# Kernel tuning notes

Hardware: AMD Instinct MI355X
Metric: run time of the kernel (lower is better)

Reference implementation:

```python
import jax, jax.numpy as jnp
import numpy as np

# 8 corner offsets of the trilinear cell: (8, 3)
_OFFS = jnp.array([[i, j, k] for i in (0, 1) for j in (0, 1) for k in (0, 1)], dtype=jnp.int32)


def _gridding(cloud, R):
    """Trilinear scatter of points into an RxRxR occupancy-weight grid.

    cloud: (b, n, 3) with coords in [-0.5, 0.5] (already divided by scale).
    Returns (b, R, R, R) grid where each point adds trilinear weights to its
    8 neighboring cells (the GRNet gridding_distance forward kernel).
    """
    b, n, _ = cloud.shape
    v = (cloud + 0.5) * R                      # continuous voxel coords in [0, R)
    lower = jnp.floor(v)
    frac = v - lower                           # (b, n, 3) in [0, 1)
    lower = lower.astype(jnp.int32)
    nb = lower[:, :, None, :] + _OFFS[None, None]              # (b, n, 8, 3)
    # per-axis trilinear weight: (1 - frac) for the low corner, frac for the high
    w_d = jnp.where(_OFFS[None, None] == 0,
                    1.0 - frac[:, :, None, :], frac[:, :, None, :])  # (b, n, 8, 3)
    w = jnp.prod(w_d, axis=-1)                                  # (b, n, 8)
    valid = jnp.all((nb >= 0) & (nb < R), axis=-1)              # (b, n, 8)
    w = jnp.where(valid, w, 0.0)
    nbc = jnp.clip(nb, 0, R - 1)
    flat = (nbc[..., 0] * R + nbc[..., 1]) * R + nbc[..., 2]    # (b, n, 8)
    batch_off = jnp.arange(b, dtype=jnp.int32)[:, None, None] * (R * R * R)
    idx = (flat + batch_off).reshape(-1)
    grid = jnp.zeros((b * R * R * R,), cloud.dtype).at[idx].add(w.reshape(-1))
    return grid.reshape(b, R, R, R)


def setup_inputs() -> dict:
    key = jax.random.key(0)
    k1, k2 = jax.random.split(key)
    R = 128
    B, N1, N2 = 16, 65536, 65536
    # coords in [-(R-2)/2, (R-2)/2] so that after /scale they are inside (-0.5, 0.5)
    pred = (jax.random.uniform(k1, (B, N1, 3), jnp.float32) - 0.5) * (R - 2)
    gt = (jax.random.uniform(k2, (B, N2, 3), jnp.float32) - 0.5) * (R - 2)
    return {"pred_cloud": pred, "gt_cloud": gt, "scale": R}


def reference(pred_cloud, gt_cloud, scale):
    pred = pred_cloud / scale
    gt = gt_cloud / scale
    return _gridding(pred, scale), _gridding(gt, scale)
```

## Files before the change

kernel.cpp:

```cpp
#include <hip/hip_runtime.h>
#include <stdint.h>


constexpr int R    = 128;
constexpr int R3c  = R * R * R;
constexpr int BPG  = 256;
constexpr int NBLK = 512;
constexpr int BLKT = 512;
constexpr int CAP  = 4096;
constexpr int MAXBINS = 8192;

constexpr size_t WS_CNT    = 0;
constexpr size_t WS_BUCKET = 1u << 20;

typedef float f4v __attribute__((ext_vector_type(4)));

__device__ __forceinline__ uint32_t quant1(float p) {
    const float S = 16384.0f;
    const uint32_t QMAX = (126u << 14) | 16383u;
    float v = p + 64.0f;
    return min(__float2uint_rn(fmaxf(v, 0.0f) * S), QMAX);
}

__device__ __forceinline__ uint2 pack_rec(uint32_t xq, uint32_t yq, uint32_t zq) {
    return make_uint2(xq | (yq << 21), (yq >> 11) | (zq << 10));
}
__device__ __forceinline__ void unpack_rec(uint2 r, uint32_t& xq, uint32_t& yq, uint32_t& zq) {
    xq = r.x & 0x1FFFFFu;
    yq = (r.x >> 21) | ((r.y & 0x3FFu) << 11);
    zq = (r.y >> 10) & 0x1FFFFFu;
}

__device__ __forceinline__ void load_point(
    const float* __restrict__ pred, const float* __restrict__ gt,
    int i, int total1, int n1, int n2, int B,
    float& px, float& py, float& pz, int& cb)
{
    const float* p;
    if (i < total1) { p = pred + (size_t)i * 3; cb = i / n1; }
    else { int j = i - total1; p = gt + (size_t)j * 3; cb = B + j / n2; }
    px = p[0]; py = p[1]; pz = p[2];
}

__device__ __forceinline__ void region_range(uint32_t xq, uint32_t yq, uint32_t zq,
                                             int& rx0, int& rx1, int& ry0, int& ry1,
                                             int& rz0, int& rz1)
{
    int ix = xq >> 14, iy = yq >> 14, iz = zq >> 14;
    rx0 = ix >> 4; rx1 = (ix + 1) >> 4;
    ry0 = iy >> 4; ry1 = (iy + 1) >> 4;
    rz0 = iz >> 5; rz1 = (iz + 1) >> 5;
}

__global__ __launch_bounds__(BLKT) void scatter_direct(
    const float* __restrict__ pred, const float* __restrict__ gt,
    int total1, int P, int n1, int n2, int B, int ppb, int vec4ok,
    uint32_t* __restrict__ cnt, uint2* __restrict__ bucket)
{
    int s = blockIdx.x * ppb, e = min(s + ppb, P);
    if (vec4ok) {
        bool isgt = (s >= total1);
        const float* src = isgt ? gt + (size_t)(s - total1) * 3
                                : pred + (size_t)s * 3;
        const int n = isgt ? n2 : n1;
        const int cb0 = isgt ? B : 0;
        const int loff = isgt ? total1 : 0;
        const float4* src4 = (const float4*)src;
        int ngrp = (e - s) >> 2;
        for (int g = threadIdx.x; g < ngrp; g += BLKT) {
            float4 a = src4[g * 3 + 0];
            float4 b4 = src4[g * 3 + 1];
            float4 c4 = src4[g * 3 + 2];
            int li = (s + g * 4) - loff;
            int hbase = (cb0 + li / n) * BPG;
            float xs[4] = {a.x, a.w, b4.z, c4.y};
            float ys[4] = {a.y, b4.x, b4.w, c4.z};
            float zs[4] = {a.z, b4.y, c4.x, c4.w};
            #pragma unroll
            for (int q = 0; q < 4; ++q) {
                uint32_t xq = quant1(xs[q]), yq = quant1(ys[q]), zq = quant1(zs[q]);
                uint2 rec = pack_rec(xq, yq, zq);
                int rx0, rx1, ry0, ry1, rz0, rz1;
                region_range(xq, yq, zq, rx0, rx1, ry0, ry1, rz0, rz1);
                for (int aa = rx0; aa <= rx1; ++aa)
                    for (int bb = ry0; bb <= ry1; ++bb)
                        for (int cc = rz0; cc <= rz1; ++cc) {
                            int bin = hbase + (aa << 5) + (bb << 2) + cc;
                            uint32_t slot = atomicAdd(&cnt[bin], 1u);
                            if (slot < (uint32_t)CAP)
                                bucket[(size_t)bin * CAP + slot] = rec;
                        }
            }
        }
    } else {
        for (int i = s + threadIdx.x; i < e; i += BLKT) {
            float px, py, pz; int cb;
            load_point(pred, gt, i, total1, n1, n2, B, px, py, pz, cb);
            uint32_t xq = quant1(px), yq = quant1(py), zq = quant1(pz);
            uint2 rec = pack_rec(xq, yq, zq);
            int rx0, rx1, ry0, ry1, rz0, rz1;
            region_range(xq, yq, zq, rx0, rx1, ry0, ry1, rz0, rz1);
            int base = cb * BPG;
            for (int a = rx0; a <= rx1; ++a)
                for (int b = ry0; b <= ry1; ++b)
                    for (int c = rz0; c <= rz1; ++c) {
                        int bin = base + (a << 5) + (b << 2) + c;
                        uint32_t slot = atomicAdd(&cnt[bin], 1u);
                        if (slot < (uint32_t)CAP)
                            bucket[(size_t)bin * CAP + slot] = rec;
                    }
        }
    }
}

__global__ __launch_bounds__(256) void accum_kernel(
    const uint32_t* __restrict__ cnt, const uint2* __restrict__ bucket,
    float* __restrict__ out)
{
    __shared__ float tile[16 * 16 * 32];
    int bin = blockIdx.x;
    int cb = bin >> 8;
    int region = bin & 255;
    int rx = region >> 5, ry = (region >> 2) & 7, rz = region & 3;

    float4* t4 = (float4*)tile;
    for (int t = threadIdx.x; t < 2048; t += 256)
        t4[t] = make_float4(0.f, 0.f, 0.f, 0.f);
    __syncthreads();

    uint32_t e = min(cnt[bin], (uint32_t)CAP);
    const uint2* recs = bucket + (size_t)bin * CAP;
    const float FQ = 6.103515625e-05f;
    for (uint32_t r = threadIdx.x; r < e; r += 256) {
        uint32_t xq, yq, zq;
        unpack_rec(recs[r], xq, yq, zq);
        int ix = xq >> 14, iy = yq >> 14, iz = zq >> 14;
        float fx = (float)(xq & 16383u) * FQ;
        float fy = (float)(yq & 16383u) * FQ;
        float fz = (float)(zq & 16383u) * FQ;
        float wx[2] = {1.0f - fx, fx};
        float wy[2] = {1.0f - fy, fy};
        float wz[2] = {1.0f - fz, fz};
        #pragma unroll
        for (int dx = 0; dx < 2; ++dx) {
            int cx = ix + dx;
            if ((cx >> 4) != rx) continue;
            #pragma unroll
            for (int dy = 0; dy < 2; ++dy) {
                int cy = iy + dy;
                if ((cy >> 4) != ry) continue;
                float wxy = wx[dx] * wy[dy];
                #pragma unroll
                for (int dz = 0; dz < 2; ++dz) {
                    int cz = iz + dz;
                    if ((cz >> 5) != rz) continue;
                    atomicAdd(&tile[(((cx & 15) << 4) + (cy & 15)) * 32 + (cz & 31)],
                              wxy * wz[dz]);
                }
            }
        }
    }
    __syncthreads();

    float* gout = out + (size_t)cb * R3c;
    for (int w = threadIdx.x; w < 2048; w += 256) {
        int lin = w * 4;
        int lx = lin >> 9, rem = lin & 511, ly = rem >> 5, lz = rem & 31;
        int X = rx * 16 + lx, Y = ry * 16 + ly, Z = rz * 32 + lz;
        f4v v = ((const f4v*)tile)[w];
        __builtin_nontemporal_store(v, (f4v*)&gout[((size_t)X * R + Y) * R + Z]);
    }
}

__device__ __forceinline__ void point_math_f(float px, float py, float pz,
                                             int& ix, int& iy, int& iz,
                                             float& fx, float& fy, float& fz)
{
    const float inv = 1.0f / 128.0f;
    float vx = (px * inv + 0.5f) * 128.0f;
    float vy = (py * inv + 0.5f) * 128.0f;
    float vz = (pz * inv + 0.5f) * 128.0f;
    float lx = floorf(vx), ly = floorf(vy), lz = floorf(vz);
    fx = vx - lx; fy = vy - ly; fz = vz - lz;
    ix = min(max((int)lx, 0), R - 2);
    iy = min(max((int)ly, 0), R - 2);
    iz = min(max((int)lz, 0), R - 2);
}

__global__ __launch_bounds__(256) void gridding_scatter(
    const float* __restrict__ cloud, float* __restrict__ grid,
    int total_pts, int n_per_batch)
{
    int idx = blockIdx.x * blockDim.x + threadIdx.x;
    if (idx >= total_pts) return;
    int b = idx / n_per_batch;
    const float* p = cloud + (size_t)idx * 3;
    int ix, iy, iz; float fx, fy, fz;
    point_math_f(p[0], p[1], p[2], ix, iy, iz, fx, fy, fz);
    float wx[2] = {1.0f - fx, fx};
    float wy[2] = {1.0f - fy, fy};
    float wz[2] = {1.0f - fz, fz};
    float* gb = grid + (size_t)b * R3c;
    #pragma unroll
    for (int dx = 0; dx < 2; ++dx)
        #pragma unroll
        for (int dy = 0; dy < 2; ++dy) {
            float wxy = wx[dx] * wy[dy];
            #pragma unroll
            for (int dz = 0; dz < 2; ++dz)
                atomicAdd(gb + ((size_t)(ix + dx) * R + (iy + dy)) * R + (iz + dz),
                          wxy * wz[dz]);
        }
}

extern "C" void kernel_launch(void* const* d_in, const int* in_sizes, int n_in,
                              void* d_out, int out_size, void* d_ws, size_t ws_size,
                              hipStream_t stream) {
    const float* pred = (const float*)d_in[0];
    const float* gt   = (const float*)d_in[1];
    float* out = (float*)d_out;

    int total1 = in_sizes[0] / 3;
    int total2 = in_sizes[1] / 3;
    int B  = out_size / (2 * R3c);
    int n1 = total1 / B;
    int n2 = total2 / B;
    int NBINS = 2 * B * BPG;
    int P  = total1 + total2;
    int ppb = (P + NBLK - 1) / NBLK;

    size_t ws_need = WS_BUCKET + (size_t)NBINS * CAP * 8;
    if (ws_size < ws_need || NBINS > MAXBINS || NBINS % 256 != 0) {
        hipMemsetAsync(d_out, 0, (size_t)out_size * sizeof(float), stream);
        gridding_scatter<<<(total1 + 255) / 256, 256, 0, stream>>>(pred, out, total1, n1);
        gridding_scatter<<<(total2 + 255) / 256, 256, 0, stream>>>(
            gt, out + (size_t)B * R3c, total2, n2);
        return;
    }

    int vec4ok = (ppb % 4 == 0) && (total1 % ppb == 0) && (P % ppb == 0) &&
                 (n1 % 4 == 0) && (n2 % 4 == 0);

    uint32_t* cnt    = (uint32_t*)((char*)d_ws + WS_CNT);
    uint2*    bucket = (uint2*)((char*)d_ws + WS_BUCKET);

    hipMemsetAsync(cnt, 0, (size_t)NBINS * sizeof(uint32_t), stream);
    scatter_direct<<<NBLK, BLKT, 0, stream>>>(pred, gt, total1, P, n1, n2, B, ppb,
                                              vec4ok, cnt, bucket);
    accum_kernel<<<NBINS, 256, 0, stream>>>(cnt, bucket, out);
}
```

Before: 406.9 us.

## Replace global-atomic bucketing with block-local counting sort and segmented accumulation

The point binning stage no longer does global atomics into fixed-capacity per-region buckets. Each block now counts its points per region in shared memory, runs a prefix scan, and writes its records into a private region-sorted segment. The accumulation kernel then gathers each region's records across all producing blocks, using per-block offsets and a binary search over segments. This removes global atomic contention, the count memset, and the capacity-overflow risk, at the cost of extra histogram and prefix arrays and an indirect gather in the accumulate step.

Result: faster. 364.7 us (-10.4%).

```diff
diff --git a/kernel.cpp b/kernel.cpp
--- a/kernel.cpp
+++ b/kernel.cpp
@@ -7,11 +7,13 @@
 constexpr int BPG  = 256;
 constexpr int NBLK = 512;
 constexpr int BLKT = 512;
-constexpr int CAP  = 4096;
-constexpr int MAXBINS = 8192;
-
-constexpr size_t WS_CNT    = 0;
-constexpr size_t WS_BUCKET = 1u << 20;
+constexpr int PPT  = 8;
+constexpr int MAXB = 128;
+constexpr int MAXSEG = 64;
+
+constexpr size_t WS_HIST = 0;
+constexpr size_t WS_PFX  = 1u << 20;
+constexpr size_t WS_REC  = 2u << 20;
 
 typedef float f4v __attribute__((ext_vector_type(4)));
 
@@ -31,17 +33,6 @@
     zq = (r.y >> 10) & 0x1FFFFFu;
 }
 
-__device__ __forceinline__ void load_point(
-    const float* __restrict__ pred, const float* __restrict__ gt,
-    int i, int total1, int n1, int n2, int B,
-    float& px, float& py, float& pz, int& cb)
-{
-    const float* p;
-    if (i < total1) { p = pred + (size_t)i * 3; cb = i / n1; }
-    else { int j = i - total1; p = gt + (size_t)j * 3; cb = B + j / n2; }
-    px = p[0]; py = p[1]; pz = p[2];
-}
-
 __device__ __forceinline__ void region_range(uint32_t xq, uint32_t yq, uint32_t zq,
                                              int& rx0, int& rx1, int& ry0, int& ry1,
                                              int& rz0, int& rz1)
@@ -52,88 +43,127 @@
     rz0 = iz >> 5; rz1 = (iz + 1) >> 5;
 }
 
-__global__ __launch_bounds__(BLKT) void scatter_direct(
+__global__ __launch_bounds__(BLKT) void sort_local(
     const float* __restrict__ pred, const float* __restrict__ gt,
-    int total1, int P, int n1, int n2, int B, int ppb, int vec4ok,
-    uint32_t* __restrict__ cnt, uint2* __restrict__ bucket)
-{
-    int s = blockIdx.x * ppb, e = min(s + ppb, P);
-    if (vec4ok) {
-        bool isgt = (s >= total1);
-        const float* src = isgt ? gt + (size_t)(s - total1) * 3
-                                : pred + (size_t)s * 3;
-        const int n = isgt ? n2 : n1;
-        const int cb0 = isgt ? B : 0;
-        const int loff = isgt ? total1 : 0;
-        const float4* src4 = (const float4*)src;
-        int ngrp = (e - s) >> 2;
-        for (int g = threadIdx.x; g < ngrp; g += BLKT) {
-            float4 a = src4[g * 3 + 0];
-            float4 b4 = src4[g * 3 + 1];
-            float4 c4 = src4[g * 3 + 2];
-            int li = (s + g * 4) - loff;
-            int hbase = (cb0 + li / n) * BPG;
-            float xs[4] = {a.x, a.w, b4.z, c4.y};
-            float ys[4] = {a.y, b4.x, b4.w, c4.z};
-            float zs[4] = {a.z, b4.y, c4.x, c4.w};
-            #pragma unroll
-            for (int q = 0; q < 4; ++q) {
-                uint32_t xq = quant1(xs[q]), yq = quant1(ys[q]), zq = quant1(zs[q]);
-                uint2 rec = pack_rec(xq, yq, zq);
-                int rx0, rx1, ry0, ry1, rz0, rz1;
-                region_range(xq, yq, zq, rx0, rx1, ry0, ry1, rz0, rz1);
-                for (int aa = rx0; aa <= rx1; ++aa)
-                    for (int bb = ry0; bb <= ry1; ++bb)
-                        for (int cc = rz0; cc <= rz1; ++cc) {
-                            int bin = hbase + (aa << 5) + (bb << 2) + cc;
-                            uint32_t slot = atomicAdd(&cnt[bin], 1u);
-                            if (slot < (uint32_t)CAP)
-                                bucket[(size_t)bin * CAP + slot] = rec;
-                        }
-            }
-        }
-    } else {
-        for (int i = s + threadIdx.x; i < e; i += BLKT) {
-            float px, py, pz; int cb;
-            load_point(pred, gt, i, total1, n1, n2, B, px, py, pz, cb);
-            uint32_t xq = quant1(px), yq = quant1(py), zq = quant1(pz);
-            uint2 rec = pack_rec(xq, yq, zq);
+    int total1, int capb,
+    uint32_t* __restrict__ hist, uint32_t* __restrict__ pfxg,
+    uint2* __restrict__ records)
+{
+    __shared__ uint32_t h[BPG];
+    __shared__ uint32_t px[BPG];
+    if (threadIdx.x < BPG) h[threadIdx.x] = 0;
+    __syncthreads();
+
+    const int ppb = PPT * BLKT;
+    int s = blockIdx.x * ppb;
+    bool isgt = (s >= total1);
+    const float4* src4 = (const float4*)(isgt ? gt + (size_t)(s - total1) * 3
+                                              : pred + (size_t)s * 3);
+    uint2 lrec[PPT / 4][4];
+    #pragma unroll
+    for (int it = 0; it < PPT / 4; ++it) {
+        int g = threadIdx.x + it * BLKT;
+        float4 a  = src4[g * 3 + 0];
+        float4 b4 = src4[g * 3 + 1];
+        float4 c4 = src4[g * 3 + 2];
+        float xs[4] = {a.x, a.w, b4.z, c4.y};
+        float ys[4] = {a.y, b4.x, b4.w, c4.z};
+        float zs[4] = {a.z, b4.y, c4.x, c4.w};
+        #pragma unroll
+        for (int q = 0; q < 4; ++q) {
+            uint32_t xq = quant1(xs[q]), yq = quant1(ys[q]), zq = quant1(zs[q]);
+            lrec[it][q] = pack_rec(xq, yq, zq);
             int rx0, rx1, ry0, ry1, rz0, rz1;
             region_range(xq, yq, zq, rx0, rx1, ry0, ry1, rz0, rz1);
-            int base = cb * BPG;
-            for (int a = rx0; a <= rx1; ++a)
-                for (int b = ry0; b <= ry1; ++b)
-                    for (int c = rz0; c <= rz1; ++c) {
-                        int bin = base + (a << 5) + (b << 2) + c;
-                        uint32_t slot = atomicAdd(&cnt[bin], 1u);
-                        if (slot < (uint32_t)CAP)
-                            bucket[(size_t)bin * CAP + slot] = rec;
+            for (int aa = rx0; aa <= rx1; ++aa)
+                for (int bb = ry0; bb <= ry1; ++bb)
+                    for (int cc = rz0; cc <= rz1; ++cc)
+                        atomicAdd(&h[(aa << 5) + (bb << 2) + cc], 1u);
+        }
+    }
+    __syncthreads();
+
+    if (threadIdx.x < BPG) px[threadIdx.x] = h[threadIdx.x];
+    __syncthreads();
+    #pragma unroll
+    for (int off = 1; off < BPG; off <<= 1) {
+        uint32_t v = 0;
+        if (threadIdx.x < BPG && threadIdx.x >= (uint32_t)off)
+            v = px[threadIdx.x - off];
+        __syncthreads();
+        if (threadIdx.x < BPG) px[threadIdx.x] += v;
+        __syncthreads();
+    }
+    if (threadIdx.x < BPG) {
+        uint32_t excl = px[threadIdx.x] - h[threadIdx.x];
+        hist[(size_t)blockIdx.x * BPG + threadIdx.x] = h[threadIdx.x];
+        pfxg[(size_t)blockIdx.x * BPG + threadIdx.x] = excl;
+        px[threadIdx.x] = excl;
+    }
+    __syncthreads();
+
+    uint2* rbase = records + (size_t)blockIdx.x * capb;
+    #pragma unroll
+    for (int it = 0; it < PPT / 4; ++it) {
+        #pragma unroll
+        for (int q = 0; q < 4; ++q) {
+            uint2 rec = lrec[it][q];
+            uint32_t xq, yq, zq;
+            unpack_rec(rec, xq, yq, zq);
+            int rx0, rx1, ry0, ry1, rz0, rz1;
+            region_range(xq, yq, zq, rx0, rx1, ry0, ry1, rz0, rz1);
+            for (int aa = rx0; aa <= rx1; ++aa)
+                for (int bb = ry0; bb <= ry1; ++bb)
+                    for (int cc = rz0; cc <= rz1; ++cc) {
+                        uint32_t slot = atomicAdd(&px[(aa << 5) + (bb << 2) + cc], 1u);
+                        rbase[slot] = rec;
                     }
         }
     }
 }
 
-__global__ __launch_bounds__(256) void accum_kernel(
-    const uint32_t* __restrict__ cnt, const uint2* __restrict__ bucket,
-    float* __restrict__ out)
+__global__ __launch_bounds__(256) void accum_seg(
+    const uint32_t* __restrict__ hist, const uint32_t* __restrict__ pfxg,
+    const uint2* __restrict__ records, float* __restrict__ out,
+    int B, int nb1, int bpg1, int bpg2, int capb)
 {
     __shared__ float tile[16 * 16 * 32];
+    __shared__ uint32_t sOff[MAXSEG + 1];
+    __shared__ uint32_t sStart[MAXSEG];
     int bin = blockIdx.x;
     int cb = bin >> 8;
-    int region = bin & 255;
-    int rx = region >> 5, ry = (region >> 2) & 7, rz = region & 3;
+    int l  = bin & 255;
+    int rx = l >> 5, ry = (l >> 2) & 7, rz = l & 3;
+
+    int first = (cb < B) ? cb * bpg1 : nb1 + (cb - B) * bpg2;
+    int cnt   = (cb < B) ? bpg1 : bpg2;
 
     float4* t4 = (float4*)tile;
     for (int t = threadIdx.x; t < 2048; t += 256)
         t4[t] = make_float4(0.f, 0.f, 0.f, 0.f);
-    __syncthreads();
-
-    uint32_t e = min(cnt[bin], (uint32_t)CAP);
-    const uint2* recs = bucket + (size_t)bin * CAP;
+    if (threadIdx.x < (uint32_t)cnt) {
+        sStart[threadIdx.x] = pfxg[(size_t)(first + threadIdx.x) * BPG + l];
+        sOff[threadIdx.x]   = hist[(size_t)(first + threadIdx.x) * BPG + l];
+    }
+    __syncthreads();
+    if (threadIdx.x == 0) {
+        uint32_t run = 0;
+        for (int k = 0; k < cnt; ++k) { uint32_t c = sOff[k]; sOff[k] = run; run += c; }
+        sOff[cnt] = run;
+    }
+    __syncthreads();
+
+    uint32_t total = sOff[cnt];
     const float FQ = 6.103515625e-05f;
-    for (uint32_t r = threadIdx.x; r < e; r += 256) {
+    for (uint32_t r = threadIdx.x; r < total; r += 256) {
+        int lo = 0, hi = cnt - 1;
+        while (lo < hi) {
+            int mid = (lo + hi + 1) >> 1;
+            if (sOff[mid] <= r) lo = mid; else hi = mid - 1;
+        }
+        uint2 rc = records[(size_t)(first + lo) * capb + sStart[lo] + (r - sOff[lo])];
         uint32_t xq, yq, zq;
-        unpack_rec(recs[r], xq, yq, zq);
+        unpack_rec(rc, xq, yq, zq);
         int ix = xq >> 14, iy = yq >> 14, iz = zq >> 14;
         float fx = (float)(xq & 16383u) * FQ;
         float fy = (float)(yq & 16383u) * FQ;
@@ -223,14 +253,22 @@
     int total1 = in_sizes[0] / 3;
     int total2 = in_sizes[1] / 3;
     int B  = out_size / (2 * R3c);
-    int n1 = total1 / B;
-    int n2 = total2 / B;
+    int n1 = (B > 0) ? total1 / B : 0;
+    int n2 = (B > 0) ? total2 / B : 0;
     int NBINS = 2 * B * BPG;
     int P  = total1 + total2;
-    int ppb = (P + NBLK - 1) / NBLK;
-
-    size_t ws_need = WS_BUCKET + (size_t)NBINS * CAP * 8;
-    if (ws_size < ws_need || NBINS > MAXBINS || NBINS % 256 != 0) {
+    int ppb = PPT * BLKT;
+
+    int capb = 8 * ppb;
+    size_t ws_need = WS_REC + (size_t)NBLK * capb * 8;
+
+    bool fastok = (B > 0) && (B <= MAXB) && (n1 > 0) && (n2 > 0) &&
+                  (total1 == B * n1) && (total2 == B * n2) &&
+                  (P == NBLK * ppb) &&
+                  (n1 % ppb == 0) && (n2 % ppb == 0) &&
+                  (n1 / ppb <= MAXSEG) && (n2 / ppb <= MAXSEG) &&
+                  (ws_size >= ws_need);
+    if (!fastok) {
         hipMemsetAsync(d_out, 0, (size_t)out_size * sizeof(float), stream);
         gridding_scatter<<<(total1 + 255) / 256, 256, 0, stream>>>(pred, out, total1, n1);
         gridding_scatter<<<(total2 + 255) / 256, 256, 0, stream>>>(
@@ -238,14 +276,15 @@
         return;
     }
 
-    int vec4ok = (ppb % 4 == 0) && (total1 % ppb == 0) && (P % ppb == 0) &&
-                 (n1 % 4 == 0) && (n2 % 4 == 0);
-
-    uint32_t* cnt    = (uint32_t*)((char*)d_ws + WS_CNT);
-    uint2*    bucket = (uint2*)((char*)d_ws + WS_BUCKET);
-
-    hipMemsetAsync(cnt, 0, (size_t)NBINS * sizeof(uint32_t), stream);
-    scatter_direct<<<NBLK, BLKT, 0, stream>>>(pred, gt, total1, P, n1, n2, B, ppb,
-                                              vec4ok, cnt, bucket);
-    accum_kernel<<<NBINS, 256, 0, stream>>>(cnt, bucket, out);
-}
+    uint32_t* hist = (uint32_t*)((char*)d_ws + WS_HIST);
+    uint32_t* pfxg = (uint32_t*)((char*)d_ws + WS_PFX);
+    uint2*    recs = (uint2*)((char*)d_ws + WS_REC);
+
+    int nb1  = total1 / ppb;
+    int bpg1 = n1 / ppb;
+    int bpg2 = n2 / ppb;
+
+    sort_local<<<NBLK, BLKT, 0, stream>>>(pred, gt, total1, capb, hist, pfxg, recs);
+    accum_seg<<<NBINS, 256, 0, stream>>>(hist, pfxg, recs, out,
+                                         B, nb1, bpg1, bpg2, capb);
+}
```
